# Optimization experiments

Measured on AMD Instinct MI355X. Metric: run time of the kernel, lower is better.

## Reference

```python
import jax, jax.numpy as jnp
import numpy as np

CLP_K = 9
SCL_KS = (3, 4, 3)  # scl0_k, scl1_k, scl2_k from the source


def _ste(f, x):
    # straight-through estimator: forward f(x), identity gradient
    return x + jax.lax.stop_gradient(f(x) - x)


def floor_ste(x):
    return _ste(jnp.floor, x)


def round_ste(x):
    return _ste(jnp.round, x)


def conv_t(x, w, b):
    # torch F.conv_transpose2d with kernel 5, stride 2, padding 2, output_padding 1
    # expressed as an lhs-dilated conv; w is torch layout [in, out, kh, kw]
    k = w.shape[-1]
    wc = jnp.flip(w, axis=(-2, -1)).transpose(1, 0, 2, 3)  # -> [out, in, kh, kw]
    lo = k - 1 - 2           # k-1-padding = 2
    hi = k - 1 - 2 + 1       # + output_padding = 3
    y = jax.lax.conv_general_dilated(
        x, wc, window_strides=(1, 1), padding=[(lo, hi), (lo, hi)],
        lhs_dilation=(2, 2), dimension_numbers=('NCHW', 'OIHW', 'NCHW'))
    return y + b[None, :, None, None]


def split_deconv(x, w, b, split):
    # sum of `split` transposed convs with floor((round(W)+j)/split) quantized weights
    out = 0.0
    for j in range(split):
        wj = floor_ste((round_ste(w) + j) / split)
        bj = floor_ste((round_ste(b) + j) / split)
        out = out + conv_t(x, wj, bj)
    return out


def _g_s_forward(x, ws, bs, ms, relus, dv, Bits, split):
    # clp[i] = round((2^Bits - 1) / relus[i] * 2^(16+clp_k))
    clp = jnp.round((2.0 ** Bits - 1.0) / relus * 2.0 ** (16 + CLP_K))
    for i in range(3):
        x = split_deconv(x, ws[i], bs[i], split)
        x = x * ms[i][None, :, None, None]
        x = floor_ste((x + 2.0 ** (dv[i] - 1 - CLP_K)) / 2.0 ** (dv[i] - CLP_K))
        x = jnp.clip(x, 0.0, clp[i])
        sk = SCL_KS[i]
        scl = floor_ste((relus[i] + 2.0 ** (sk - 1)) / 2.0 ** sk)
        x = floor_ste((x * scl + 2.0 ** (15 + CLP_K - sk)) / 2.0 ** (16 + CLP_K - sk))
    x = split_deconv(x, ws[3], bs[3], split)
    x = x * ms[3][None, :, None, None]
    x = floor_ste((x + 2.0 ** (dv[3] - 9)) / 2.0 ** (dv[3] - 8))
    return x / 255.0


def setup_inputs() -> dict:
    key = jax.random.key(0)
    ks = jax.random.split(key, 16)
    N, M = 192, 320
    B, h, w = 1, 48, 48
    x = jax.random.randint(ks[0], (B, M, h, w), 0, 256).astype(jnp.float32)
    w1 = jax.random.normal(ks[1], (M, N, 5, 5), jnp.float32) * 20.0
    b1 = jax.random.normal(ks[2], (N,), jnp.float32) * 20.0
    w2 = jax.random.normal(ks[3], (N, N, 5, 5), jnp.float32) * 20.0
    b2 = jax.random.normal(ks[4], (N,), jnp.float32) * 20.0
    w3 = jax.random.normal(ks[5], (N, N, 5, 5), jnp.float32) * 20.0
    b3 = jax.random.normal(ks[6], (N,), jnp.float32) * 20.0
    w4 = jax.random.normal(ks[7], (N, 3, 5, 5), jnp.float32) * 20.0
    b4 = jax.random.normal(ks[8], (3,), jnp.float32) * 20.0
    muls0 = jax.random.randint(ks[9], (N,), 1, 1000).astype(jnp.float32)
    muls1 = jax.random.randint(ks[10], (N,), 1, 1000).astype(jnp.float32)
    muls2 = jax.random.randint(ks[11], (N,), 1, 1000).astype(jnp.float32)
    muls3 = jax.random.randint(ks[12], (3,), 1, 1000).astype(jnp.float32)
    relus = jnp.array([40000.0, 36000.0, 30000.0], jnp.float32)
    muls_dvds = jnp.array([24, 24, 24, 24], jnp.int32)
    return {"x": x, "w1": w1, "b1": b1, "w2": w2, "b2": b2, "w3": w3,
            "b3": b3, "w4": w4, "b4": b4, "muls0": muls0, "muls1": muls1,
            "muls2": muls2, "muls3": muls3, "relus": relus,
            "muls_dvds": muls_dvds, "Bits": 8, "split": 4}


def reference(x, w1, b1, w2, b2, w3, b3, w4, b4,
              muls0, muls1, muls2, muls3, relus, muls_dvds, Bits, split):
    dv = muls_dvds.astype(jnp.float32)
    ws = (w1, w2, w3, w4)
    bs = (b1, b2, b3, b4)
    ms = (muls0, muls1, muls2, muls3)
    return _g_s_forward(x, ws, bs, ms, relus, dv, int(Bits), int(split))
```

## Files before the change

### kernel.cpp

```cpp
#include <hip/hip_runtime.h>
#include <cmath>


typedef int int4v  __attribute__((ext_vector_type(4)));
typedef int int16v __attribute__((ext_vector_type(16)));

__device__ __forceinline__ void tap_to_k(int t, int& ky, int& kx) {
    if (t < 9)       { int dy = t/3,  dx = t%3;                   ky = 4-2*dy; kx = 4-2*dx; }
    else if (t < 15) { int u = t-9;   int dy = u/2, dx = 1+(u&1);  ky = 4-2*dy; kx = 5-2*dx; }
    else if (t < 21) { int u = t-15;  int dy = 1+u/3, dx = u%3;    ky = 5-2*dy; kx = 4-2*dx; }
    else             { int u = t-21;  int dy = 1+u/2, dx = 1+(u&1); ky = 5-2*dy; kx = 5-2*dx; }
}

__global__ __launch_bounds__(256)
void convert_x_t(const float* __restrict__ x, signed char* __restrict__ xh,
                 int C, int HW) {
    __shared__ float t[64][65];
    const int p0 = blockIdx.x * 64;
    const int c0 = blockIdx.y * 64;
    const int pL = threadIdx.x & 63;
    const int r0 = threadIdx.x >> 6;
    #pragma unroll
    for (int k = 0; k < 16; ++k) {
        int ciL = r0 * 16 + k;
        t[ciL][pL] = x[(size_t)(c0 + ciL) * HW + p0 + pL];
    }
    __syncthreads();
    #pragma unroll
    for (int k = 0; k < 16; ++k) {
        int pL2 = r0 * 16 + k;
        xh[(size_t)(p0 + pL2) * C + c0 + pL] = (signed char)((int)t[pL][pL2] - 128);
    }
}

__global__ __launch_bounds__(256)
void pack3(const float* __restrict__ w1, const float* __restrict__ w2,
           const float* __restrict__ w3,
           signed char* __restrict__ p1, signed char* __restrict__ p2,
           signed char* __restrict__ p3) {
    const int layer = blockIdx.y;
    const float* w = (layer == 0) ? w1 : (layer == 1) ? w2 : w3;
    signed char* out = (layer == 0) ? p1 : (layer == 1) ? p2 : p3;
    const int Cin = (layer == 0) ? 320 : 192;
    const int Cout = 192, NT = 6;
    int idx = blockIdx.x * 256 + threadIdx.x;
    if (idx >= Cin * Cout) return;
    const int co = idx % Cout, ci = idx / Cout;
    const float* wr = w + (size_t)(ci * Cout + co) * 25;
    float v[25];
    #pragma unroll
    for (int k = 0; k < 25; ++k) {
        float t = rintf(wr[k]);
        v[k] = fminf(fmaxf(t, -128.0f), 127.0f);
    }
    const int qs = ci >> 5, half = (ci >> 4) & 1, j = ci & 15;
    const int nb = co >> 5, lane = half * 32 + (co & 31);
    size_t base = ((size_t)(qs * NT + nb) * 25) * 1024 + lane * 16 + j;
    #pragma unroll
    for (int t = 0; t < 25; ++t) {
        int ky, kx; tap_to_k(t, ky, kx);
        out[base + (size_t)t * 1024] = (signed char)(int)v[ky * 5 + kx];
    }
}

__global__ void pack_w4_i8(const float* __restrict__ w, signed char* __restrict__ wpk) {
    int idx = blockIdx.x * blockDim.x + threadIdx.x;
    if (idx >= 6 * 9 * 64 * 16) return;
    int j    = idx & 15;
    int lane = (idx >> 4) & 63;
    int rem  = idx >> 10;
    int s9   = rem % 9;
    int qs   = rem / 9;
    int col  = lane & 31;
    int co   = col & 7;
    int p    = col >> 3;
    int py = p >> 1, px = p & 1;
    int dy = s9 / 3, dx = s9 % 3;
    int ci = qs * 32 + ((lane >> 5) << 4) + j;
    bool part = (py == 0 || dy >= 1) && (px == 0 || dx >= 1);
    float v = 0.0f;
    if (co < 3 && part) {
        int ky = py ? 5 - 2 * dy : 4 - 2 * dy;
        int kx = px ? 5 - 2 * dx : 4 - 2 * dx;
        v = rintf(w[(size_t)(ci * 3 + co) * 25 + ky * 5 + kx]);
        v = fminf(fmaxf(v, -128.0f), 127.0f);
    }
    wpk[idx] = (signed char)(int)v;
}

__global__ __launch_bounds__(64)
void tap4(const float* __restrict__ w1, const float* __restrict__ w2,
          const float* __restrict__ w3, const float* __restrict__ w4,
          int* __restrict__ t1, int* __restrict__ t2,
          int* __restrict__ t3, int* __restrict__ t4) {
    const int layer = blockIdx.y;
    const float* w = (layer == 0) ? w1 : (layer == 1) ? w2 : (layer == 2) ? w3 : w4;
    int* ts = (layer == 0) ? t1 : (layer == 1) ? t2 : (layer == 2) ? t3 : t4;
    const int Cin = (layer == 0) ? 320 : 192;
    const int Cout = (layer == 3) ? 3 : 192;
    const int i = blockIdx.x;
    if (i >= 4 * Cout) return;
    const int co = i % Cout, p = i / Cout;
    const int py = p >> 1, px = p & 1;
    const int nky = (5 - py + 1) >> 1;
    const int nkx = (5 - px + 1) >> 1;
    const int ntap = nky * nkx;
    int s = 0;
    for (int idx = threadIdx.x; idx < Cin * ntap; idx += 64) {
        const int ci = idx / ntap;
        const int u  = idx - ci * ntap;
        const int ky = py + 2 * (u / nkx);
        const int kx = px + 2 * (u % nkx);
        float v = rintf(w[(size_t)(ci * Cout + co) * 25 + ky * 5 + kx]);
        v = fminf(fmaxf(v, -128.0f), 127.0f);
        s += (int)v;
    }
    #pragma unroll
    for (int off = 32; off > 0; off >>= 1)
        s += __shfl_down(s, off, 64);
    if (threadIdx.x == 0) ts[i] = s;
}

__device__ __constant__ const int S_NT[9]     = {1,2,2,2,4,4,2,4,4};
__device__ __constant__ const int S_TAP[9][4] = {
    {0,0,0,0},{1,9,0,0},{2,10,0,0},{3,15,0,0},
    {4,11,16,21},{5,12,17,22},{6,18,0,0},{7,13,19,23},{8,14,20,24}};
__device__ __constant__ const int S_PAR[9][4] = {
    {0,0,0,0},{0,1,0,0},{0,1,0,0},{0,2,0,0},
    {0,1,2,3},{0,1,2,3},{0,2,0,0},{0,1,2,3},{0,1,2,3}};

template<int MW>
__global__ __launch_bounds__(MW * 64)
void deconv_v6(const signed char* __restrict__ xin, const signed char* __restrict__ wpk,
               const float* __restrict__ bias, const float* __restrict__ muls,
               const int* __restrict__ tsum,
               const float* __restrict__ relus, const int* __restrict__ dvds,
               const int* __restrict__ bitsp,
               int layer, int Cin, int Cout, int NT, int Hq, int Wq,
               signed char* __restrict__ outp) {
    constexpr int R = 2;
    constexpr int NROW = MW * R * 2 + 2;
    constexpr int NPIX = NROW * 18;
    constexpr int THREADS = MW * 64;
    constexpr int XC = NPIX * 2;
    constexpr int XI = (XC + THREADS - 1) / THREADS;
    constexpr int BC = 1600;
    constexpr int BI = (BC + THREADS - 1) / THREADS;

    __shared__ __align__(16) signed char xs[NPIX * 48];
    __shared__ __align__(16) signed char bs[25600];

    const int tid  = threadIdx.x;
    const int lane = tid & 63;
    const int wid  = tid >> 6;
    const int qx0  = blockIdx.y * 16;
    const int qy0  = blockIdx.z * (MW * R * 2);
    const int nb   = blockIdx.x;
    const int n0   = nb * 32;

    int16v acc[R][4];
    #pragma unroll
    for (int r = 0; r < R; ++r)
        #pragma unroll
        for (int p = 0; p < 4; ++p)
            #pragma unroll
            for (int e = 0; e < 16; ++e) acc[r][p][e] = 0;

    const int half   = lane >> 5;
    const int rowbit = (lane >> 4) & 1;
    const int col    = lane & 15;
    int p0[R];
    #pragma unroll
    for (int r = 0; r < R; ++r)
        p0[r] = ((wid * R + r) * 2 + rowbit) * 18 + col;

    int4v xreg[XI], breg[BI];

    auto load_chunk = [&](int ck) {
        const signed char* wslab = wpk + (size_t)((ck >> 5) * NT + nb) * 25600;
        #pragma unroll
        for (int t = 0; t < XI; ++t) {
            int i = tid + t * THREADS;
            if (i < XC) {
                int pix = i >> 1, g = i & 1;
                int rr = pix / 18, cc = pix - rr * 18;
                int y = qy0 - 1 + rr, xx = qx0 - 1 + cc;
                int4v v = {(int)0x80808080, (int)0x80808080,
                           (int)0x80808080, (int)0x80808080};
                if ((unsigned)y < (unsigned)Hq && (unsigned)xx < (unsigned)Wq)
                    v = *(const int4v*)&xin[((size_t)y * Wq + xx) * Cin + ck + g * 16];
                xreg[t] = v;
            }
        }
        #pragma unroll
        for (int t = 0; t < BI; ++t) {
            int i = tid + t * THREADS;
            if (i < BC) breg[t] = *(const int4v*)&wslab[(size_t)i * 16];
        }
    };
    auto store_chunk = [&]() {
        #pragma unroll
        for (int t = 0; t < XI; ++t) {
            int i = tid + t * THREADS;
            if (i < XC) {
                int pix = i >> 1, g = i & 1;
                *(int4v*)&xs[pix * 48 + g * 16] = xreg[t];
            }
        }
        #pragma unroll
        for (int t = 0; t < BI; ++t) {
            int i = tid + t * THREADS;
            if (i < BC) *(int4v*)&bs[i * 16] = breg[t];
        }
    };

    load_chunk(0);
    for (int ck = 0; ck < Cin; ck += 32) {
        __syncthreads();
        store_chunk();
        __syncthreads();
        if (ck + 32 < Cin) load_chunk(ck + 32);

        #pragma unroll
        for (int s9 = 0; s9 < 9; ++s9) {
            const int dy = s9 / 3, dx = s9 % 3;
            int4v a[R];
            #pragma unroll
            for (int r = 0; r < R; ++r)
                a[r] = *(const int4v*)&xs[(p0[r] + dy * 18 + dx) * 48 + half * 16];
            #pragma unroll
            for (int u = 0; u < 4; ++u) {
                if (u < S_NT[s9]) {
                    int4v b = *(const int4v*)&bs[S_TAP[s9][u] * 1024 + lane * 16];
                    const int p = S_PAR[s9][u];
                    #pragma unroll
                    for (int r = 0; r < R; ++r)
                        acc[r][p] = __builtin_amdgcn_mfma_i32_32x32x32_i8(a[r], b, acc[r][p], 0, 0, 0);
                }
            }
        }
    }

    const int dv = dvds[layer];
    float add1 = ldexpf(1.0f, dv - 10);
    float inv1 = ldexpf(1.0f, -(dv - 9));
    const float relu = relus[layer];
    const int sk = (layer == 1) ? 4 : 3;
    const float bitsv = ldexpf(1.0f, bitsp[0]) - 1.0f;
    float clp, scl;
    {
        #pragma clang fp contract(off)
        clp = rintf(bitsv / relu * 33554432.0f);
        scl = floorf((relu + ldexpf(1.0f, sk - 1)) * ldexpf(1.0f, -sk));
    }
    float add2 = ldexpf(1.0f, 24 - sk);
    float inv2 = ldexpf(1.0f, -(25 - sk));

    const int co = n0 + (lane & 31);
    float bq = rintf(bias[co]);
    float mm = muls[co];
    int fullp[4];
    #pragma unroll
    for (int p = 0; p < 4; ++p) fullp[p] = tsum[p * Cout + co];

    const int Wout = Wq * 2;

    #pragma unroll
    for (int r = 0; r < R; ++r) {
        #pragma unroll
        for (int p = 0; p < 4; ++p) {
            const int py = p >> 1, px = p & 1;
            #pragma unroll
            for (int reg = 0; reg < 16; ++reg) {
                const int mrow = (reg & 3) + 8 * (reg >> 2) + 4 * (lane >> 5);
                const int qy = qy0 + (wid * R + r) * 2 + (mrow >> 4);
                const int qx = qx0 + (mrow & 15);
                float v = (float)(acc[r][p][reg] + 128 * fullp[p]);
                {
                    #pragma clang fp contract(off)
                    v = (v + bq) * mm;
                    v = floorf((v + add1) * inv1);
                    v = fminf(fmaxf(v, 0.0f), clp);
                    v = floorf((v * scl + add2) * inv2);
                }
                const int oy = 2 * qy + py, ox = 2 * qx + px;
                outp[((size_t)oy * Wout + ox) * Cout + co] = (signed char)((int)v - 128);
            }
        }
    }
}

__global__ __launch_bounds__(512)
void deconv_final_v6(const signed char* __restrict__ xin, const signed char* __restrict__ wpk,
                     const float* __restrict__ bias, const float* __restrict__ muls,
                     const int* __restrict__ tsum, const int* __restrict__ dvds,
                     int Cin, int Hq, int Wq, float* __restrict__ outp) {
    constexpr int R = 2, MW = 8;
    constexpr int NROW = MW * R * 2 + 2;
    constexpr int NPIX = NROW * 18;
    constexpr int THREADS = 512;
    constexpr int XC = NPIX * 2;
    constexpr int XI = (XC + THREADS - 1) / THREADS;
    constexpr int BC = 576;
    constexpr int BI = (BC + THREADS - 1) / THREADS;

    __shared__ __align__(16) signed char xs[NPIX * 48];
    __shared__ __align__(16) signed char bs[9216];

    const int tid  = threadIdx.x;
    const int lane = tid & 63;
    const int wid  = tid >> 6;
    const int qx0  = blockIdx.y * 16;
    const int qy0  = blockIdx.z * (MW * R * 2);

    int16v acc[R];
    #pragma unroll
    for (int r = 0; r < R; ++r)
        #pragma unroll
        for (int e = 0; e < 16; ++e) acc[r][e] = 0;

    const int half   = lane >> 5;
    const int rowbit = (lane >> 4) & 1;
    const int col    = lane & 15;
    int p0[R];
    #pragma unroll
    for (int r = 0; r < R; ++r)
        p0[r] = ((wid * R + r) * 2 + rowbit) * 18 + col;

    int4v xreg[XI], breg[BI];

    auto load_chunk = [&](int ck) {
        const signed char* wslab = wpk + (size_t)(ck >> 5) * 9216;
        #pragma unroll
        for (int t = 0; t < XI; ++t) {
            int i = tid + t * THREADS;
            if (i < XC) {
                int pix = i >> 1, g = i & 1;
                int rr = pix / 18, cc = pix - rr * 18;
                int y = qy0 - 1 + rr, xx = qx0 - 1 + cc;
                int4v v = {(int)0x80808080, (int)0x80808080,
                           (int)0x80808080, (int)0x80808080};
                if ((unsigned)y < (unsigned)Hq && (unsigned)xx < (unsigned)Wq)
                    v = *(const int4v*)&xin[((size_t)y * Wq + xx) * Cin + ck + g * 16];
                xreg[t] = v;
            }
        }
        #pragma unroll
        for (int t = 0; t < BI; ++t) {
            int i = tid + t * THREADS;
            if (i < BC) breg[t] = *(const int4v*)&wslab[(size_t)i * 16];
        }
    };
    auto store_chunk = [&]() {
        #pragma unroll
        for (int t = 0; t < XI; ++t) {
            int i = tid + t * THREADS;
            if (i < XC) {
                int pix = i >> 1, g = i & 1;
                *(int4v*)&xs[pix * 48 + g * 16] = xreg[t];
            }
        }
        #pragma unroll
        for (int t = 0; t < BI; ++t) {
            int i = tid + t * THREADS;
            if (i < BC) *(int4v*)&bs[i * 16] = breg[t];
        }
    };

    load_chunk(0);
    for (int ck = 0; ck < Cin; ck += 32) {
        __syncthreads();
        store_chunk();
        __syncthreads();
        if (ck + 32 < Cin) load_chunk(ck + 32);

        #pragma unroll
        for (int s9 = 0; s9 < 9; ++s9) {
            const int dy = s9 / 3, dx = s9 % 3;
            int4v b = *(const int4v*)&bs[s9 * 1024 + lane * 16];
            #pragma unroll
            for (int r = 0; r < R; ++r) {
                int4v a = *(const int4v*)&xs[(p0[r] + dy * 18 + dx) * 48 + half * 16];
                acc[r] = __builtin_amdgcn_mfma_i32_32x32x32_i8(a, b, acc[r], 0, 0, 0);
            }
        }
    }

    const int dv = dvds[3];
    const float add1 = ldexpf(1.0f, dv - 9);
    const float inv1 = ldexpf(1.0f, -(dv - 8));

    const int coln = lane & 31;
    const int co = coln & 7;
    const int p  = coln >> 3;
    const int py = p >> 1, px = p & 1;
    const bool valid = (co < 3);
    float bq = 0.f, mm = 0.f;
    int fp = 0;
    if (valid) { bq = rintf(bias[co]); mm = muls[co]; fp = tsum[p * 3 + co]; }

    const int Wout = Wq * 2, Hout = Hq * 2;
    #pragma unroll
    for (int r = 0; r < R; ++r) {
        #pragma unroll
        for (int reg = 0; reg < 16; ++reg) {
            const int mrow = (reg & 3) + 8 * (reg >> 2) + 4 * (lane >> 5);
            const int qy = qy0 + (wid * R + r) * 2 + (mrow >> 4);
            const int qx = qx0 + (mrow & 15);
            float v = (float)(acc[r][reg] + 128 * fp);
            {
                #pragma clang fp contract(off)
                v = (v + bq) * mm;
                v = floorf((v + add1) * inv1);
                v = v / 255.0f;
            }
            if (valid) {
                const int oy = 2 * qy + py, ox = 2 * qx + px;
                outp[((size_t)co * Hout + oy) * Wout + ox] = v;
            }
        }
    }
}

extern "C" void kernel_launch(void* const* d_in, const int* in_sizes, int n_in,
                              void* d_out, int out_size, void* d_ws, size_t ws_size,
                              hipStream_t stream) {
    const float* x  = (const float*)d_in[0];
    const float* w1 = (const float*)d_in[1];
    const float* b1 = (const float*)d_in[2];
    const float* w2 = (const float*)d_in[3];
    const float* b2 = (const float*)d_in[4];
    const float* w3 = (const float*)d_in[5];
    const float* b3 = (const float*)d_in[6];
    const float* w4 = (const float*)d_in[7];
    const float* b4 = (const float*)d_in[8];
    const float* m0 = (const float*)d_in[9];
    const float* m1 = (const float*)d_in[10];
    const float* m2 = (const float*)d_in[11];
    const float* m3 = (const float*)d_in[12];
    const float* relus = (const float*)d_in[13];
    const int* dvds = (const int*)d_in[14];
    const int* bitsp = (const int*)d_in[15];

    signed char* wsb = (signed char*)d_ws;
    size_t o = 0;
    signed char* wpk1 = wsb + o; o += (size_t)10 * 6 * 25600;
    signed char* wpk2 = wsb + o; o += (size_t)6 * 6 * 25600;
    signed char* wpk3 = wsb + o; o += (size_t)6 * 6 * 25600;
    signed char* wpk4 = wsb + o; o += (size_t)6 * 9216;
    int* ts1 = (int*)(wsb + o); o += 4 * 192 * 4;
    int* ts2 = (int*)(wsb + o); o += 4 * 192 * 4;
    int* ts3 = (int*)(wsb + o); o += 4 * 192 * 4;
    int* ts4 = (int*)(wsb + o); o += 4 * 4 * 4;
    o = (o + 15) & ~(size_t)15;
    signed char* xh = wsb + o; o += (size_t)48 * 48 * 320;
    signed char* a1 = wsb + o; o += (size_t)96 * 96 * 192;
    signed char* a2 = wsb + o; o += (size_t)192 * 192 * 192;
    signed char* a3 = wsb + o; o += (size_t)384 * 384 * 192;

    convert_x_t<<<dim3(36, 5), 256, 0, stream>>>(x, xh, 320, 48 * 48);
    pack3<<<dim3(240, 3), 256, 0, stream>>>(w1, w2, w3, wpk1, wpk2, wpk3);
    pack_w4_i8<<<(6 * 9 * 1024 + 255) / 256, 256, 0, stream>>>(w4, wpk4);
    tap4<<<dim3(768, 4), 64, 0, stream>>>(w1, w2, w3, w4, ts1, ts2, ts3, ts4);

    deconv_v6<4><<<dim3(6, 3, 3), 256, 0, stream>>>(
        xh, wpk1, b1, m0, ts1, relus, dvds, bitsp, 0, 320, 192, 6, 48, 48, a1);
    deconv_v6<4><<<dim3(6, 6, 6), 256, 0, stream>>>(
        a1, wpk2, b2, m1, ts2, relus, dvds, bitsp, 1, 192, 192, 6, 96, 96, a2);
    deconv_v6<8><<<dim3(6, 12, 6), 512, 0, stream>>>(
        a2, wpk3, b3, m2, ts3, relus, dvds, bitsp, 2, 192, 192, 6, 192, 192, a3);
    deconv_final_v6<<<dim3(1, 24, 12), 512, 0, stream>>>(
        a3, wpk4, b4, m3, ts4, dvds, 192, 384, 384, (float*)d_out);
}
```

Measured before the change: 235.6 us.

## Split output parities across wave pairs to halve accumulators per wave

Each pair of waves now shares a spatial tile, with one wave computing parity planes 0 and 3 and the other computing planes 1 and 2. This halves the accumulator registers per wave and balances the MFMA count between the two roles (10 taps and 15 taps split evenly). Launch bounds gain a min-blocks hint of 3, and grids are doubled to cover the smaller per-block tile. The cost is more blocks that each reload the shared weight slab, and duplicate activation LDS reads within a pair.

```diff
diff --git a/kernel.cpp b/kernel.cpp
--- a/kernel.cpp
+++ b/kernel.cpp
@@ -121,17 +121,50 @@
     if (threadIdx.x == 0) ts[i] = s;
 }
 
-__device__ __constant__ const int S_NT[9]     = {1,2,2,2,4,4,2,4,4};
-__device__ __constant__ const int S_TAP[9][4] = {
-    {0,0,0,0},{1,9,0,0},{2,10,0,0},{3,15,0,0},
-    {4,11,16,21},{5,12,17,22},{6,18,0,0},{7,13,19,23},{8,14,20,24}};
-__device__ __constant__ const int S_PAR[9][4] = {
-    {0,0,0,0},{0,1,0,0},{0,1,0,0},{0,2,0,0},
-    {0,1,2,3},{0,1,2,3},{0,2,0,0},{0,1,2,3},{0,1,2,3}};
+__device__ __forceinline__ constexpr int role_nt(int role, int s9) {
+    constexpr int NT0[9] = {1,1,1,1,2,2,1,2,2};
+    constexpr int NT1[9] = {0,1,1,1,2,2,1,2,2};
+    return role == 0 ? NT0[s9] : NT1[s9];
+}
+__device__ __forceinline__ constexpr int role_tap(int role, int s9, int u) {
+    constexpr int T0[9][2] = {{0,0},{1,0},{2,0},{3,0},{4,21},{5,22},{6,0},{7,23},{8,24}};
+    constexpr int T1[9][2] = {{0,0},{9,0},{10,0},{15,0},{11,16},{12,17},{18,0},{13,19},{14,20}};
+    return role == 0 ? T0[s9][u] : T1[s9][u];
+}
+__device__ __forceinline__ constexpr int role_acc(int role, int s9, int u) {
+    constexpr int A0[9][2] = {{0,0},{0,0},{0,0},{0,0},{0,1},{0,1},{0,0},{0,1},{0,1}};
+    constexpr int A1[9][2] = {{0,0},{0,0},{0,0},{1,0},{0,1},{0,1},{1,0},{0,1},{0,1}};
+    return role == 0 ? A0[s9][u] : A1[s9][u];
+}
+
+template<int ROLE, int R>
+__device__ __forceinline__ void compute_role(const signed char* xs, const signed char* bs,
+                                             int16v (&acc)[R][2], const int (&p0)[R],
+                                             int half, int lane) {
+    #pragma unroll
+    for (int s9 = 0; s9 < 9; ++s9) {
+        if (role_nt(ROLE, s9) == 0) continue;
+        const int dy = s9 / 3, dx = s9 % 3;
+        int4v a[R];
+        #pragma unroll
+        for (int r = 0; r < R; ++r)
+            a[r] = *(const int4v*)&xs[(p0[r] + dy * 18 + dx) * 48 + half * 16];
+        #pragma unroll
+        for (int u = 0; u < 2; ++u) {
+            if (u < role_nt(ROLE, s9)) {
+                int4v b = *(const int4v*)&bs[role_tap(ROLE, s9, u) * 1024 + lane * 16];
+                const int ai = role_acc(ROLE, s9, u);
+                #pragma unroll
+                for (int r = 0; r < R; ++r)
+                    acc[r][ai] = __builtin_amdgcn_mfma_i32_32x32x32_i8(a[r], b, acc[r][ai], 0, 0, 0);
+            }
+        }
+    }
+}
 
 template<int MW>
-__global__ __launch_bounds__(MW * 64)
-void deconv_v6(const signed char* __restrict__ xin, const signed char* __restrict__ wpk,
+__global__ __launch_bounds__(MW * 64, 3)
+void deconv_v7(const signed char* __restrict__ xin, const signed char* __restrict__ wpk,
                const float* __restrict__ bias, const float* __restrict__ muls,
                const int* __restrict__ tsum,
                const float* __restrict__ relus, const int* __restrict__ dvds,
@@ -139,7 +172,8 @@
                int layer, int Cin, int Cout, int NT, int Hq, int Wq,
                signed char* __restrict__ outp) {
     constexpr int R = 2;
-    constexpr int NROW = MW * R * 2 + 2;
+    constexpr int PAIRS = MW / 2;
+    constexpr int NROW = PAIRS * R * 2 + 2;
     constexpr int NPIX = NROW * 18;
     constexpr int THREADS = MW * 64;
     constexpr int XC = NPIX * 2;
@@ -153,16 +187,18 @@
     const int tid  = threadIdx.x;
     const int lane = tid & 63;
     const int wid  = tid >> 6;
+    const int pairId = wid >> 1;
+    const int role   = wid & 1;
     const int qx0  = blockIdx.y * 16;
-    const int qy0  = blockIdx.z * (MW * R * 2);
+    const int qy0  = blockIdx.z * (PAIRS * R * 2);
     const int nb   = blockIdx.x;
     const int n0   = nb * 32;
 
-    int16v acc[R][4];
+    int16v acc[R][2];
     #pragma unroll
     for (int r = 0; r < R; ++r)
         #pragma unroll
-        for (int p = 0; p < 4; ++p)
+        for (int p = 0; p < 2; ++p)
             #pragma unroll
             for (int e = 0; e < 16; ++e) acc[r][p][e] = 0;
 
@@ -172,7 +208,7 @@
     int p0[R];
     #pragma unroll
     for (int r = 0; r < R; ++r)
-        p0[r] = ((wid * R + r) * 2 + rowbit) * 18 + col;
+        p0[r] = ((pairId * R + r) * 2 + rowbit) * 18 + col;
 
     int4v xreg[XI], breg[BI];
 
@@ -221,24 +257,8 @@
         __syncthreads();
         if (ck + 32 < Cin) load_chunk(ck + 32);
 
-        #pragma unroll
-        for (int s9 = 0; s9 < 9; ++s9) {
-            const int dy = s9 / 3, dx = s9 % 3;
-            int4v a[R];
-            #pragma unroll
-            for (int r = 0; r < R; ++r)
-                a[r] = *(const int4v*)&xs[(p0[r] + dy * 18 + dx) * 48 + half * 16];
-            #pragma unroll
-            for (int u = 0; u < 4; ++u) {
-                if (u < S_NT[s9]) {
-                    int4v b = *(const int4v*)&bs[S_TAP[s9][u] * 1024 + lane * 16];
-                    const int p = S_PAR[s9][u];
-                    #pragma unroll
-                    for (int r = 0; r < R; ++r)
-                        acc[r][p] = __builtin_amdgcn_mfma_i32_32x32x32_i8(a[r], b, acc[r][p], 0, 0, 0);
-                }
-            }
-        }
+        if (role == 0) compute_role<0, R>(xs, bs, acc, p0, half, lane);
+        else           compute_role<1, R>(xs, bs, acc, p0, half, lane);
     }
 
     const int dv = dvds[layer];
@@ -259,23 +279,27 @@
     const int co = n0 + (lane & 31);
     float bq = rintf(bias[co]);
     float mm = muls[co];
-    int fullp[4];
-    #pragma unroll
-    for (int p = 0; p < 4; ++p) fullp[p] = tsum[p * Cout + co];
+    int pmap[2];
+    pmap[0] = role == 0 ? 0 : 1;
+    pmap[1] = role == 0 ? 3 : 2;
+    int fullp[2];
+    #pragma unroll
+    for (int a = 0; a < 2; ++a) fullp[a] = tsum[pmap[a] * Cout + co];
 
     const int Wout = Wq * 2;
 
     #pragma unroll
     for (int r = 0; r < R; ++r) {
         #pragma unroll
-        for (int p = 0; p < 4; ++p) {
+        for (int a = 0; a < 2; ++a) {
+            const int p = pmap[a];
             const int py = p >> 1, px = p & 1;
             #pragma unroll
             for (int reg = 0; reg < 16; ++reg) {
                 const int mrow = (reg & 3) + 8 * (reg >> 2) + 4 * (lane >> 5);
-                const int qy = qy0 + (wid * R + r) * 2 + (mrow >> 4);
+                const int qy = qy0 + (pairId * R + r) * 2 + (mrow >> 4);
                 const int qx = qx0 + (mrow & 15);
-                float v = (float)(acc[r][p][reg] + 128 * fullp[p]);
+                float v = (float)(acc[r][a][reg] + 128 * fullp[a]);
                 {
                     #pragma clang fp contract(off)
                     v = (v + bq) * mm;
@@ -290,8 +314,8 @@
     }
 }
 
-__global__ __launch_bounds__(512)
-void deconv_final_v6(const signed char* __restrict__ xin, const signed char* __restrict__ wpk,
+__global__ __launch_bounds__(512, 3)
+void deconv_final_v7(const signed char* __restrict__ xin, const signed char* __restrict__ wpk,
                      const float* __restrict__ bias, const float* __restrict__ muls,
                      const int* __restrict__ tsum, const int* __restrict__ dvds,
                      int Cin, int Hq, int Wq, float* __restrict__ outp) {
@@ -463,12 +487,12 @@
     pack_w4_i8<<<(6 * 9 * 1024 + 255) / 256, 256, 0, stream>>>(w4, wpk4);
     tap4<<<dim3(768, 4), 64, 0, stream>>>(w1, w2, w3, w4, ts1, ts2, ts3, ts4);
 
-    deconv_v6<4><<<dim3(6, 3, 3), 256, 0, stream>>>(
+    deconv_v7<4><<<dim3(6, 3, 6), 256, 0, stream>>>(
         xh, wpk1, b1, m0, ts1, relus, dvds, bitsp, 0, 320, 192, 6, 48, 48, a1);
-    deconv_v6<4><<<dim3(6, 6, 6), 256, 0, stream>>>(
+    deconv_v7<8><<<dim3(6, 6, 6), 512, 0, stream>>>(
         a1, wpk2, b2, m1, ts2, relus, dvds, bitsp, 1, 192, 192, 6, 96, 96, a2);
-    deconv_v6<8><<<dim3(6, 12, 6), 512, 0, stream>>>(
+    deconv_v7<8><<<dim3(6, 12, 12), 512, 0, stream>>>(
         a2, wpk3, b3, m2, ts3, relus, dvds, bitsp, 2, 192, 192, 6, 192, 192, a3);
-    deconv_final_v6<<<dim3(1, 24, 12), 512, 0, stream>>>(
+    deconv_final_v7<<<dim3(1, 24, 12), 512, 0, stream>>>(
         a3, wpk4, b4, m3, ts4, dvds, 192, 384, 384, (float*)d_out);
 }
```

After: 224.4 us. 1.05x faster.
